# Optimization experiments

Measured on AMD Instinct MI355X. Metric: run time of the kernel, lower is better.

## Reference

```python
import jax, jax.numpy as jnp
import numpy as np

B, NQ, C, H, W, S1, S2 = 8, 100, 256, 64, 64, 7, 7
G = S1 * S2


def setup_inputs() -> dict:
    key = jax.random.key(0)
    ks = iter(jax.random.split(key, 64))
    rn = lambda shape, s=1.0: jax.random.normal(next(ks), shape, dtype=jnp.float32) * s
    d = {}
    d['q'] = rn((B, NQ, C))
    d['qpe'] = rn((B, NQ, C)) * 0.1
    d['feat'] = rn((B, C, H, W))
    d['feat_pe'] = rn((B, C, H, W)) * 0.1
    d['bboxes'] = jax.random.uniform(next(ks), (B, NQ, 4), dtype=jnp.float32)
    d['grid_embedding'] = rn((S1, S2, C), 0.02)
    for name in ['Wz', 'Wq', 'W1l', 'W2l', 'g1_w1', 'g1_w2', 'g2_w1', 'g2_w2',
                 'f1_w1', 'f1_w2', 'f2_w1', 'f2_w2', 'out_w']:
        d[name] = rn((C, C), 0.06)  # ~xavier for 256->256
    for name in ['bz', 'bq', 'b1l', 'b2l', 'g1_b1', 'g1_b2', 'g2_b1', 'g2_b2',
                 'f1_b1', 'f1_b2', 'f2_b1', 'f2_b2', 'out_b', 'g1_beta', 'g2_beta', 'out_beta']:
        d[name] = jnp.zeros((C,), jnp.float32)
    for name in ['g1_g', 'g2_g', 'out_g']:
        d[name] = jnp.ones((C,), jnp.float32)
    return d


def _ln(x, g, b):
    m = jnp.mean(x, -1, keepdims=True)
    v = jnp.mean((x - m) ** 2, -1, keepdims=True)
    return (x - m) * jax.lax.rsqrt(v + 1e-5) * g + b


def _mlp(x, w1, b1, w2, b2):  # 2-layer MLP: relu after first layer only
    return jax.nn.relu(x @ w1 + b1) @ w2 + b2


def _bilinear(img, gx, gy):
    # img: [B,C,H,W]; gx,gy: [B,P] in [-1,1]. torch grid_sample bilinear,
    # align_corners=False, zeros padding.
    Bb, Cc, Hh, Ww = img.shape
    ix = ((gx + 1.0) * Ww - 1.0) * 0.5
    iy = ((gy + 1.0) * Hh - 1.0) * 0.5
    x0 = jnp.floor(ix); x1 = x0 + 1.0
    y0 = jnp.floor(iy); y1 = y0 + 1.0
    wx1 = ix - x0; wx0 = 1.0 - wx1
    wy1 = iy - y0; wy0 = 1.0 - wy1
    flat = img.reshape(Bb, Cc, Hh * Ww)

    def tap(xf, yf):
        xi = xf.astype(jnp.int32); yi = yf.astype(jnp.int32)
        valid = (xi >= 0) & (xi < Ww) & (yi >= 0) & (yi < Hh)
        idx = jnp.clip(yi, 0, Hh - 1) * Ww + jnp.clip(xi, 0, Ww - 1)
        v = jnp.take_along_axis(flat, idx[:, None, :], axis=2)  # [B,C,P]
        return v * valid[:, None, :].astype(img.dtype)

    return (tap(x0, y0) * (wx0 * wy0)[:, None, :]
            + tap(x1, y0) * (wx1 * wy0)[:, None, :]
            + tap(x0, y1) * (wx0 * wy1)[:, None, :]
            + tap(x1, y1) * (wx1 * wy1)[:, None, :])


def _roi_sample(img, bboxes):
    # img: [B,C,H,W]; bboxes: [B,nq,4] xyhw -> returns [B,nq,G,C]
    Bb, Cc, Hh, Ww = img.shape
    nq = bboxes.shape[1]
    hs = jnp.arange(S1, dtype=img.dtype)
    ws = jnp.arange(S2, dtype=img.dtype)
    h_sl = bboxes[:, :, 2:3] / S1  # [B,nq,1]
    w_sl = bboxes[:, :, 3:4] / S2
    hh = h_sl * hs[None, None, :] + h_sl / 2.0  # [B,nq,S1]
    ww = w_sl * ws[None, None, :] + w_sl / 2.0  # [B,nq,S2]
    ys = jnp.broadcast_to(hh[:, :, :, None], (Bb, nq, S1, S2))
    xs = jnp.broadcast_to(ww[:, :, None, :], (Bb, nq, S1, S2))
    xs = xs + bboxes[:, :, 0, None, None] - bboxes[:, :, 3, None, None] / 2.0
    ys = ys + bboxes[:, :, 1, None, None] - bboxes[:, :, 2, None, None] / 2.0
    gx = jnp.clip(2.0 * xs - 1.0, -1.0, 1.0).reshape(Bb, -1)
    gy = jnp.clip(2.0 * ys - 1.0, -1.0, 1.0).reshape(Bb, -1)
    s = _bilinear(img, gx, gy)  # [B,C,nq*G]
    return s.reshape(Bb, Cc, nq, G).transpose(0, 2, 3, 1)  # [B,nq,G,C]


def reference(q, qpe, feat, feat_pe, bboxes, grid_embedding,
              Wz, bz, Wq, bq, W1l, b1l, W2l, b2l,
              g1_w1, g1_b1, g1_w2, g1_b2, g1_g, g1_beta,
              g2_w1, g2_b1, g2_w2, g2_b2, g2_g, g2_beta,
              f1_w1, f1_b1, f1_w2, f1_b2,
              f2_w1, f2_b1, f2_w2, f2_b2,
              out_w, out_b, out_g, out_beta):
    ge = grid_embedding.reshape(G, C)
    q_split = ((q + qpe) @ Wq + bq)[:, :, None, :] + ge[None, None]  # [B,nq,G,C]
    # 1x1 conv conv_z
    z = jnp.einsum('bchw,cd->bdhw', feat + feat_pe, Wz) + bz[None, :, None, None]
    roi_feat = _roi_sample(z, bboxes)  # [B,nq,G,C]
    k = (q_split @ W1l + b1l) * (roi_feat @ W2l + b2l)
    q2 = q[:, :, None, :] + ge[None, None]
    v = _roi_sample(feat, bboxes)  # [B,nq,G,C]
    gate1 = jax.nn.sigmoid(_ln(_mlp(k, g1_w1, g1_b1, g1_w2, g1_b2), g1_g, g1_beta))
    gate2 = jax.nn.sigmoid(_ln(_mlp(k, g2_w1, g2_b1, g2_w2, g2_b2), g2_g, g2_beta))
    out = gate1 * _mlp(q2, f1_w1, f1_b1, f1_w2, f1_b2) + gate2 * _mlp(v, f2_w1, f2_b1, f2_w2, f2_b2)
    return _ln(out @ out_w + out_b, out_g, out_beta)
```

## Files before the change

### kernel.cpp

```cpp
#include <hip/hip_runtime.h>
#include <hip/hip_bf16.h>
#include <hip/hip_fp8.h>

constexpr int Cc  = 256;
constexpr int NQ  = 100;
constexpr int Bb  = 8;
constexpr int HW  = 64 * 64;
constexpr int G49 = 49;

typedef __bf16 bf16x8 __attribute__((ext_vector_type(8)));
typedef float  f32x4  __attribute__((ext_vector_type(4)));

__device__ __forceinline__ float ldbf(const __hip_bfloat16* p) { return __bfloat162float(*p); }

__device__ __forceinline__ unsigned pk2(float a, float b) {
    union { unsigned u; __bf16 h[2]; } x;
    x.h[0] = (__bf16)a; x.h[1] = (__bf16)b;
    return x.u;
}
__device__ __forceinline__ float upk(unsigned u, int k) {
    union { unsigned u2; __bf16 h[2]; } x; x.u2 = u;
    return (float)x.h[k];
}
__device__ __forceinline__ float fp8lo(unsigned v) {
    union { unsigned char c; __hip_fp8_e4m3 f; } u; u.c = (unsigned char)(v & 255);
    return (float)u.f;
}
__device__ __forceinline__ float fp8hi(unsigned v) {
    union { unsigned char c; __hip_fp8_e4m3 f; } u; u.c = (unsigned char)((v >> 8) & 255);
    return (float)u.f;
}

__device__ __forceinline__ void lwb16(char* buf, int row, int col, float v) {
    int byte = (row * 512 + col * 2) ^ ((row & 7) << 4);
    *(__bf16*)(buf + byte) = (__bf16)v;
}

__global__ void prep1_kernel(const float* __restrict__ q, const float* __restrict__ qpe,
                             const float* __restrict__ ge,
                             const float* __restrict__ Wq, const float* __restrict__ bq,
                             const float* __restrict__ W1l, const float* __restrict__ b1l,
                             const float* __restrict__ f1_w1, const float* __restrict__ f1_b1,
                             __hip_bfloat16* __restrict__ qk1, __hip_bfloat16* __restrict__ qf1,
                             __hip_bfloat16* __restrict__ geW1, __hip_bfloat16* __restrict__ gef1)
{
    __shared__ float s[Cc];
    __shared__ float rq[Cc];
    __shared__ float qqs[Cc];
    const int t = threadIdx.x;
    const int blk = blockIdx.x;
    if (blk < Bb * NQ) {
        float a = q[blk * Cc + t], p = qpe[blk * Cc + t];
        rq[t] = a; s[t] = a + p;
        __syncthreads();
        float acc1 = bq[t], acc2 = f1_b1[t];
        for (int k = 0; k < Cc; k++) {
            acc1 = fmaf(s[k],  Wq[k * Cc + t],    acc1);
            acc2 = fmaf(rq[k], f1_w1[k * Cc + t], acc2);
        }
        qqs[t] = acc1;
        qf1[blk * Cc + t] = __float2bfloat16(acc2);
        __syncthreads();
        float acc3 = b1l[t];
        for (int k = 0; k < Cc; k++) acc3 = fmaf(qqs[k], W1l[k * Cc + t], acc3);
        qk1[blk * Cc + t] = __float2bfloat16(acc3);
    } else {
        int g = blk - Bb * NQ;
        s[t] = ge[g * Cc + t];
        __syncthreads();
        float acc1 = 0.f, acc2 = 0.f;
        for (int k = 0; k < Cc; k++) {
            acc1 = fmaf(s[k], W1l[k * Cc + t],   acc1);
            acc2 = fmaf(s[k], f1_w1[k * Cc + t], acc2);
        }
        geW1[g * Cc + t] = __float2bfloat16(acc1);
        gef1[g * Cc + t] = __float2bfloat16(acc2);
    }
}

__global__ void wfold_kernel(const float* __restrict__ Wz, const float* __restrict__ W2l,
                             const float* __restrict__ bz,
                             float* __restrict__ Wzc, float* __restrict__ bzW2l)
{
    __shared__ float s[Cc];
    const int t = threadIdx.x;
    const int blk = blockIdx.x;
    if (blk < Cc) {
        s[t] = Wz[blk * Cc + t];
        __syncthreads();
        float a = 0.f;
        for (int d = 0; d < Cc; d++) a = fmaf(s[d], W2l[d * Cc + t], a);
        Wzc[blk * Cc + t] = a;
    } else {
        s[t] = bz[t];
        __syncthreads();
        float a = 0.f;
        for (int d = 0; d < Cc; d++) a = fmaf(s[d], W2l[d * Cc + t], a);
        bzW2l[t] = a;
    }
}

__global__ void wprep_kernel(const float* __restrict__ Wzc,  const float* __restrict__ f2w1,
                             const float* __restrict__ g2w1, const float* __restrict__ g2w2,
                             const float* __restrict__ f2w2, const float* __restrict__ g1w1,
                             const float* __restrict__ g1w2, const float* __restrict__ f1w2,
                             const float* __restrict__ outw,
                             __hip_bfloat16* __restrict__ WTf)
{
    __shared__ float ld[64][65];
    const float* srcs[9] = {Wzc, f2w1, g2w1, g2w2, f2w2, g1w1, g1w2, f1w2, outw};
    const int m  = blockIdx.z;
    const int w  = blockIdx.y;
    const int k0 = blockIdx.x * 64;
    const float* src = srcs[m];
    __hip_bfloat16* dst = WTf + (size_t)m * 65536;
    const int t = threadIdx.x;
    const int n0 = w * 64;
#pragma unroll
    for (int j = 0; j < 16; j++) {
        int idx = j * 256 + t; int r = idx >> 6, c = idx & 63;
        ld[r][c] = src[(size_t)(k0 + r) * Cc + n0 + c];
    }
    __syncthreads();
#pragma unroll
    for (int j = 0; j < 16; j++) {
        int idx = j * 256 + t;
        int e  = idx & 7;
        int l  = (idx >> 3) & 63;
        int kk = (idx >> 9) & 1;
        int nt = idx >> 10;
        int k_loc = kk * 32 + ((l >> 4) & 3) * 8 + e;
        int n_loc = nt * 16 + (l & 15);
        int oofs  = ((w * 4 + nt) * 8 + (k0 >> 5) + kk) * 512 + (idx & 511);
        dst[oofs] = __float2bfloat16(ld[k_loc][n_loc]);
    }
}

__device__ __forceinline__ void run_gemm4(const char* __restrict__ Abuf,
                                          const __bf16* __restrict__ Wf,
                                          int l15, int lhi, int lane, int w, int n0, f32x4* acc)
{
#pragma unroll
    for (int j = 0; j < 16; j++) { f32x4 v = {0.f, 0.f, 0.f, 0.f}; acc[j] = v; }
#pragma unroll
    for (int ks = 0; ks < 8; ks++) {
        bf16x8 bfr[4], afr[4];
#pragma unroll
        for (int nt = 0; nt < 4; nt++)
            bfr[nt] = *(const bf16x8*)(Wf + ((((w * 4 + nt) * 8 + ks) * 64) + lane) * 8);
#pragma unroll
        for (int mt = 0; mt < 4; mt++) {
            int row = mt * 16 + l15;
            int byte = (row * 512 + (ks * 32 + lhi * 8) * 2) ^ ((row & 7) << 4);
            afr[mt] = *(const bf16x8*)(Abuf + byte);
        }
#pragma unroll
        for (int mt = 0; mt < 4; mt++)
#pragma unroll
            for (int nt = 0; nt < 4; nt++)
                acc[mt * 4 + nt] = __builtin_amdgcn_mfma_f32_16x16x32_bf16(
                    afr[mt], bfr[nt], acc[mt * 4 + nt], 0, 0, 0);
    }
}

__global__ __launch_bounds__(256, 2) void projA_kernel(
    const float* __restrict__ feat, const float* __restrict__ feat_pe,
    const __hip_bfloat16* __restrict__ WTf,
    __hip_fp8_e4m3* __restrict__ y1, __hip_bfloat16* __restrict__ y2)
{
    extern __shared__ char smem[];
    char* bufA = smem;
    char* bufB = smem + 32768;

    const int t = threadIdx.x;
    const int lane = t & 63;
    const int w = t >> 6;
    const int n0 = w * 64;
    const int l15 = lane & 15, lhi = lane >> 4;
    const int b = blockIdx.x >> 6;
    const int pix0 = (blockIdx.x & 63) * 64;

    const float* fp = feat    + ((size_t)(b * Cc + t)) * HW + pix0;
    const float* pp = feat_pe + ((size_t)(b * Cc + t)) * HW + pix0;
#pragma unroll
    for (int j = 0; j < 16; j++) {
        float4 f = *(const float4*)(fp + 4 * j);
        float4 p = *(const float4*)(pp + 4 * j);
        lwb16(bufB, 4 * j + 0, t, f.x); lwb16(bufA, 4 * j + 0, t, f.x + p.x);
        lwb16(bufB, 4 * j + 1, t, f.y); lwb16(bufA, 4 * j + 1, t, f.y + p.y);
        lwb16(bufB, 4 * j + 2, t, f.z); lwb16(bufA, 4 * j + 2, t, f.z + p.z);
        lwb16(bufB, 4 * j + 3, t, f.w); lwb16(bufA, 4 * j + 3, t, f.w + p.w);
    }
    __syncthreads();

    const __bf16* Wf_zc   = (const __bf16*)WTf + 0 * 65536;
    const __bf16* Wf_f2w1 = (const __bf16*)WTf + 1 * 65536;

    f32x4 acc[16];
    size_t base = ((size_t)b * HW + pix0) * Cc;

    run_gemm4(bufA, Wf_zc, l15, lhi, lane, w, n0, acc);
#pragma unroll
    for (int nt = 0; nt < 4; nt++)
#pragma unroll
        for (int mt = 0; mt < 4; mt++)
#pragma unroll
            for (int i = 0; i < 4; i++)
                y1[base + (size_t)(mt * 16 + lhi * 4 + i) * Cc + n0 + nt * 16 + l15] =
                    __hip_fp8_e4m3(acc[mt * 4 + nt][i]);

    run_gemm4(bufB, Wf_f2w1, l15, lhi, lane, w, n0, acc);
#pragma unroll
    for (int nt = 0; nt < 4; nt++)
#pragma unroll
        for (int mt = 0; mt < 4; mt++)
#pragma unroll
            for (int i = 0; i < 4; i++)
                y2[base + (size_t)(mt * 16 + lhi * 4 + i) * Cc + n0 + nt * 16 + l15] =
                    __float2bfloat16(acc[mt * 4 + nt][i]);
}

__device__ __forceinline__ void run_gemm8(const char* __restrict__ Abuf,
                                          const __bf16* __restrict__ Wf,
                                          const float* __restrict__ bias,
                                          int l15, int lhi, int lane, int wm, int wn, f32x4* acc)
{
#pragma unroll
    for (int nt = 0; nt < 4; nt++) {
        float bv = bias ? bias[wn * 64 + nt * 16 + l15] : 0.f;
        f32x4 v = {bv, bv, bv, bv};
        acc[0 * 4 + nt] = v; acc[1 * 4 + nt] = v;
    }
#pragma unroll
    for (int ks = 0; ks < 8; ks++) {
        bf16x8 bfr[4], afr[2];
#pragma unroll
        for (int nt = 0; nt < 4; nt++)
            bfr[nt] = *(const bf16x8*)(Wf + ((((wn * 4 + nt) * 8 + ks) * 64) + lane) * 8);
#pragma unroll
        for (int mt = 0; mt < 2; mt++) {
            int row = wm * 32 + mt * 16 + l15;
            int byte = (row * 512 + (ks * 32 + lhi * 8) * 2) ^ ((row & 7) << 4);
            afr[mt] = *(const bf16x8*)(Abuf + byte);
        }
        __builtin_amdgcn_s_setprio(1);
#pragma unroll
        for (int mt = 0; mt < 2; mt++)
#pragma unroll
            for (int nt = 0; nt < 4; nt++)
                acc[mt * 4 + nt] = __builtin_amdgcn_mfma_f32_16x16x32_bf16(
                    afr[mt], bfr[nt], acc[mt * 4 + nt], 0, 0, 0);
        __builtin_amdgcn_s_setprio(0);
    }
}

__device__ __forceinline__ void ln_stats8(const f32x4* acc, int l15, int lhi, int wm, int wn,
                                          int t, float* sred, float* smv)
{
    __syncthreads();
    float s[8], qq[8];
#pragma unroll
    for (int mt = 0; mt < 2; mt++)
#pragma unroll
        for (int i = 0; i < 4; i++) {
            float a = acc[mt * 4 + 0][i], b = acc[mt * 4 + 1][i];
            float c = acc[mt * 4 + 2][i], d = acc[mt * 4 + 3][i];
            s[mt * 4 + i]  = a + b + c + d;
            qq[mt * 4 + i] = a * a + b * b + c * c + d * d;
        }
#pragma unroll
    for (int off = 1; off < 16; off <<= 1)
#pragma unroll
        for (int j = 0; j < 8; j++) {
            s[j]  += __shfl_xor(s[j],  off);
            qq[j] += __shfl_xor(qq[j], off);
        }
    if (l15 == 0) {
#pragma unroll
        for (int mt = 0; mt < 2; mt++)
#pragma unroll
            for (int i = 0; i < 4; i++) {
                int row = wm * 32 + mt * 16 + lhi * 4 + i;
                sred[(row * 4 + wn) * 2]     = s[mt * 4 + i];
                sred[(row * 4 + wn) * 2 + 1] = qq[mt * 4 + i];
            }
    }
    __syncthreads();
    if (t < 64) {
        float ts = sred[(t * 4 + 0) * 2] + sred[(t * 4 + 1) * 2]
                 + sred[(t * 4 + 2) * 2] + sred[(t * 4 + 3) * 2];
        float tq = sred[(t * 4 + 0) * 2 + 1] + sred[(t * 4 + 1) * 2 + 1]
                 + sred[(t * 4 + 2) * 2 + 1] + sred[(t * 4 + 3) * 2 + 1];
        float m = ts * (1.f / 256.f);
        float var = fmaxf(tq * (1.f / 256.f) - m * m, 0.f);
        smv[t * 2]     = m;
        smv[t * 2 + 1] = rsqrtf(var + 1e-5f);
    }
    __syncthreads();
}

__device__ __forceinline__ void gate_apply8(const f32x4* acc, const float* __restrict__ g,
                                            const float* __restrict__ bet, const float* smv,
                                            int l15, int lhi, int wm, int wn, unsigned* gp)
{
#pragma unroll
    for (int nt = 0; nt < 4; nt++) {
        int col = wn * 64 + nt * 16 + l15;
        float gg = g[col], gb = bet[col];
#pragma unroll
        for (int mt = 0; mt < 2; mt++) {
            float gv[4];
#pragma unroll
            for (int i = 0; i < 4; i++) {
                int row = wm * 32 + mt * 16 + lhi * 4 + i;
                float u = (acc[mt * 4 + nt][i] - smv[row * 2]) * smv[row * 2 + 1] * gg + gb;
                gv[i] = 1.f / (1.f + __expf(-u));
            }
            gp[(mt * 4 + nt) * 2]     = pk2(gv[0], gv[1]);
            gp[(mt * 4 + nt) * 2 + 1] = pk2(gv[2], gv[3]);
        }
    }
}

__global__ __launch_bounds__(512, 2) void fused_kernel(
    const float* __restrict__ bboxes,
    const __hip_bfloat16* __restrict__ qk1, const __hip_bfloat16* __restrict__ qf1,
    const __hip_bfloat16* __restrict__ geW1, const __hip_bfloat16* __restrict__ gef1,
    const __hip_fp8_e4m3* __restrict__ y1, const __hip_bfloat16* __restrict__ y2,
    const __hip_bfloat16* __restrict__ WTf,
    const float* __restrict__ bzW2l, const float* __restrict__ b2l,
    const float* __restrict__ f2_b1, const float* __restrict__ f2_b2,
    const float* __restrict__ g1_b1, const float* __restrict__ g1_b2,
    const float* __restrict__ g1_g,  const float* __restrict__ g1_beta,
    const float* __restrict__ g2_b1, const float* __restrict__ g2_b2,
    const float* __restrict__ g2_g,  const float* __restrict__ g2_beta,
    const float* __restrict__ f1_b2,
    const float* __restrict__ out_b, const float* __restrict__ out_g,
    const float* __restrict__ out_beta,
    float* __restrict__ out)
{
    extern __shared__ char smem[];
    char* bufA = smem;
    char* bufB = smem + 32768;
    float* stg = (float*)smem;

    __shared__ int   ti[G49][4];
    __shared__ float tw[G49][4];
    __shared__ float tsw[G49];
    __shared__ float sred[64 * 4 * 2];
    __shared__ float smv[64 * 2];

    const int t = threadIdx.x;
    const int lane = t & 63;
    const int w = t >> 6;
    const int wm = w >> 2, wn = w & 3;
    const int l15 = lane & 15, lhi = lane >> 4;
    const int qid = (blockIdx.x & 7) * NQ + (blockIdx.x >> 3);
    const int b = blockIdx.x & 7;

    const __bf16* Wf_g2w1 = (const __bf16*)WTf + 2 * 65536;
    const __bf16* Wf_g2w2 = (const __bf16*)WTf + 3 * 65536;
    const __bf16* Wf_f2w2 = (const __bf16*)WTf + 4 * 65536;
    const __bf16* Wf_g1w1 = (const __bf16*)WTf + 5 * 65536;
    const __bf16* Wf_g1w2 = (const __bf16*)WTf + 6 * 65536;
    const __bf16* Wf_f1w2 = (const __bf16*)WTf + 7 * 65536;
    const __bf16* Wf_outw = (const __bf16*)WTf + 8 * 65536;

    if (t < G49) {
        float bb0 = bboxes[qid * 4 + 0];
        float bb1 = bboxes[qid * 4 + 1];
        float bb2 = bboxes[qid * 4 + 2];
        float bb3 = bboxes[qid * 4 + 3];
        int s1 = t / 7, s2 = t % 7;
        float ys = bb2 * (1.f / 7.f) * ((float)s1 + 0.5f) + bb1 - 0.5f * bb2;
        float xs = bb3 * (1.f / 7.f) * ((float)s2 + 0.5f) + bb0 - 0.5f * bb3;
        float gx = fminf(fmaxf(2.f * xs - 1.f, -1.f), 1.f);
        float gy = fminf(fmaxf(2.f * ys - 1.f, -1.f), 1.f);
        float ix = ((gx + 1.f) * 64.f - 1.f) * 0.5f;
        float iy = ((gy + 1.f) * 64.f - 1.f) * 0.5f;
        float x0f = floorf(ix), y0f = floorf(iy);
        float wx1 = ix - x0f, wx0 = 1.f - wx1;
        float wy1 = iy - y0f, wy0 = 1.f - wy1;
        int x0 = (int)x0f, y0 = (int)y0f;
        int x1 = x0 + 1, y1i = y0 + 1;
        bool vx0 = (x0 >= 0) & (x0 < 64), vx1 = (x1 >= 0) & (x1 < 64);
        bool vy0 = (y0 >= 0) & (y0 < 64), vy1 = (y1i >= 0) & (y1i < 64);
        int cx0 = min(max(x0, 0), 63), cx1 = min(max(x1, 0), 63);
        int cy0 = min(max(y0, 0), 63), cy1 = min(max(y1i, 0), 63);
        float w0 = (vx0 && vy0) ? wx0 * wy0 : 0.f;
        float w1 = (vx1 && vy0) ? wx1 * wy0 : 0.f;
        float w2 = (vx0 && vy1) ? wx0 * wy1 : 0.f;
        float w3 = (vx1 && vy1) ? wx1 * wy1 : 0.f;
        ti[t][0] = cy0 * 64 + cx0; tw[t][0] = w0;
        ti[t][1] = cy0 * 64 + cx1; tw[t][1] = w1;
        ti[t][2] = cy1 * 64 + cx0; tw[t][2] = w2;
        ti[t][3] = cy1 * 64 + cx1; tw[t][3] = w3;
        tsw[t] = w0 + w1 + w2 + w3;
    }
    if (t < Cc) {
        for (int r = G49; r < 64; r++) { lwb16(bufA, r, t, 0.f); lwb16(bufB, r, t, 0.f); }
    }
    __syncthreads();

    {
        const __hip_fp8_e4m3* y1b = y1 + (size_t)b * HW * Cc;
        const __hip_bfloat16* y2b = y2 + (size_t)b * HW * Cc;
        const int c2 = (t & 127) * 2;
        const int rs = t >> 7;
        const float qk0  = ldbf(&qk1[qid * Cc + c2]);
        const float qk1v = ldbf(&qk1[qid * Cc + c2 + 1]);
        const float bzw0 = bzW2l[c2],  bzw1 = bzW2l[c2 + 1];
        const float b20  = b2l[c2],    b21  = b2l[c2 + 1];
        const float fb0  = f2_b1[c2],  fb1  = f2_b1[c2 + 1];
        for (int it = 0; it < 13; it++) {
            int r = it * 4 + rs;
            if (r < G49) {
                int4   tix = *(const int4*)&ti[r][0];
                float4 twx = *(const float4*)&tw[r][0];
                size_t o0 = (size_t)tix.x * Cc + c2;
                size_t o1 = (size_t)tix.y * Cc + c2;
                size_t o2 = (size_t)tix.z * Cc + c2;
                size_t o3 = (size_t)tix.w * Cc + c2;
                unsigned p0 = *(const unsigned short*)((const char*)y1b + o0);
                unsigned p1 = *(const unsigned short*)((const char*)y1b + o1);
                unsigned p2 = *(const unsigned short*)((const char*)y1b + o2);
                unsigned p3 = *(const unsigned short*)((const char*)y1b + o3);
                unsigned q0 = *(const unsigned*)(y2b + o0);
                unsigned q1 = *(const unsigned*)(y2b + o1);
                unsigned q2 = *(const unsigned*)(y2b + o2);
                unsigned q3 = *(const unsigned*)(y2b + o3);
                float a10 = fp8lo(p0) * twx.x + fp8lo(p1) * twx.y
                          + fp8lo(p2) * twx.z + fp8lo(p3) * twx.w;
                float a11 = fp8hi(p0) * twx.x + fp8hi(p1) * twx.y
                          + fp8hi(p2) * twx.z + fp8hi(p3) * twx.w;
                float a20 = upk(q0, 0) * twx.x + upk(q1, 0) * twx.y
                          + upk(q2, 0) * twx.z + upk(q3, 0) * twx.w;
                float a21 = upk(q0, 1) * twx.x + upk(q1, 1) * twx.y
                          + upk(q2, 1) * twx.z + upk(q3, 1) * twx.w;
                float ts_ = tsw[r];
                unsigned gep = *(const unsigned*)(geW1 + r * Cc + c2);
                float kv0 = (qk0  + upk(gep, 0)) * (a10 + ts_ * bzw0 + b20);
                float kv1 = (qk1v + upk(gep, 1)) * (a11 + ts_ * bzw1 + b21);
                int byteB = (r * 512 + c2 * 2) ^ ((r & 7) << 4);
                *(unsigned*)(bufB + byteB) = pk2(kv0, kv1);
                *(unsigned*)(bufA + byteB) = pk2(fmaxf(a20 + fb0, 0.f), fmaxf(a21 + fb1, 0.f));
            }
        }
    }
    __syncthreads();

    f32x4 acc[8], acc2[8];

    run_gemm8(bufA, Wf_f2w2, f2_b2, l15, lhi, lane, wm, wn, acc);
    unsigned m2p[16];
#pragma unroll
    for (int j = 0; j < 8; j++) {
        m2p[j * 2]     = pk2(acc[j][0], acc[j][1]);
        m2p[j * 2 + 1] = pk2(acc[j][2], acc[j][3]);
    }

    run_gemm8(bufB, Wf_g2w1, g2_b1, l15, lhi, lane, wm, wn, acc);
    run_gemm8(bufB, Wf_g1w1, g1_b1, l15, lhi, lane, wm, wn, acc2);
    __syncthreads();
#pragma unroll
    for (int nt = 0; nt < 4; nt++)
#pragma unroll
        for (int mt = 0; mt < 2; mt++)
#pragma unroll
            for (int i = 0; i < 4; i++) {
                int row = wm * 32 + mt * 16 + lhi * 4 + i, col = wn * 64 + nt * 16 + l15;
                lwb16(bufA, row, col, fmaxf(acc [mt * 4 + nt][i], 0.f));
                lwb16(bufB, row, col, fmaxf(acc2[mt * 4 + nt][i], 0.f));
            }
    __syncthreads();

    run_gemm8(bufA, Wf_g2w2, g2_b2, l15, lhi, lane, wm, wn, acc);
    ln_stats8(acc, l15, lhi, wm, wn, t, sred, smv);
    unsigned g2p[16];
    gate_apply8(acc, g2_g, g2_beta, smv, l15, lhi, wm, wn, g2p);
    unsigned comb[16];
#pragma unroll
    for (int j = 0; j < 16; j++)
        comb[j] = pk2(upk(g2p[j], 0) * upk(m2p[j], 0), upk(g2p[j], 1) * upk(m2p[j], 1));

    run_gemm8(bufB, Wf_g1w2, g1_b2, l15, lhi, lane, wm, wn, acc);
    ln_stats8(acc, l15, lhi, wm, wn, t, sred, smv);
    unsigned g1p[16];
    gate_apply8(acc, g1_g, g1_beta, smv, l15, lhi, wm, wn, g1p);

    {
        int col = t & 255, rh = t >> 8;
        float qf = ldbf(&qf1[qid * Cc + col]);
        for (int it = 0; it < 32; it++) {
            int r = it * 2 + rh;
            int rr = r < G49 ? r : 0;
            lwb16(bufA, r, col, fmaxf(qf + ldbf(&gef1[rr * Cc + col]), 0.f));
        }
    }
    __syncthreads();

    run_gemm8(bufA, Wf_f1w2, f1_b2, l15, lhi, lane, wm, wn, acc);
    __syncthreads();
#pragma unroll
    for (int nt = 0; nt < 4; nt++)
#pragma unroll
        for (int mt = 0; mt < 2; mt++)
#pragma unroll
            for (int i = 0; i < 4; i++) {
                int j = mt * 4 + nt;
                int hw_ = i >> 1, lo = i & 1;
                float f = upk(comb[j * 2 + hw_], lo) + upk(g1p[j * 2 + hw_], lo) * acc[j][i];
                lwb16(bufA, wm * 32 + mt * 16 + lhi * 4 + i, wn * 64 + nt * 16 + l15, f);
            }
    __syncthreads();

    run_gemm8(bufA, Wf_outw, out_b, l15, lhi, lane, wm, wn, acc);
    ln_stats8(acc, l15, lhi, wm, wn, t, sred, smv);
#pragma unroll
    for (int nt = 0; nt < 4; nt++) {
        int col = wn * 64 + nt * 16 + l15;
        float gg = out_g[col], gb = out_beta[col];
#pragma unroll
        for (int mt = 0; mt < 2; mt++)
#pragma unroll
            for (int i = 0; i < 4; i++) {
                int row = wm * 32 + mt * 16 + lhi * 4 + i;
                if (row < G49)
                    stg[row * Cc + col] =
                        (acc[mt * 4 + nt][i] - smv[row * 2]) * smv[row * 2 + 1] * gg + gb;
            }
    }
    __syncthreads();
    {
        float* ob = out + (size_t)qid * G49 * Cc;
#pragma unroll
        for (int it = 0; it < 7; it++) {
            int fid = it * 512 + t;
            int r = fid >> 6, c4 = (fid & 63) * 4;
            if (r < G49) {
                f32x4 v = *(const f32x4*)&stg[r * Cc + c4];
                *(f32x4*)&ob[r * Cc + c4] = v;
            }
        }
    }
}

extern "C" void kernel_launch(void* const* d_in, const int* in_sizes, int n_in,
                              void* d_out, int out_size, void* d_ws, size_t ws_size,
                              hipStream_t stream)
{
    const float* q       = (const float*)d_in[0];
    const float* qpe     = (const float*)d_in[1];
    const float* feat    = (const float*)d_in[2];
    const float* feat_pe = (const float*)d_in[3];
    const float* bboxes  = (const float*)d_in[4];
    const float* ge      = (const float*)d_in[5];
    const float* Wz      = (const float*)d_in[6];
    const float* Wq      = (const float*)d_in[7];
    const float* W1l     = (const float*)d_in[8];
    const float* W2l     = (const float*)d_in[9];
    const float* g1_w1   = (const float*)d_in[10];
    const float* g1_w2   = (const float*)d_in[11];
    const float* g2_w1   = (const float*)d_in[12];
    const float* g2_w2   = (const float*)d_in[13];
    const float* f1_w1   = (const float*)d_in[14];
    const float* f1_w2   = (const float*)d_in[15];
    const float* f2_w1   = (const float*)d_in[16];
    const float* f2_w2   = (const float*)d_in[17];
    const float* out_w   = (const float*)d_in[18];
    const float* bz      = (const float*)d_in[19];
    const float* bq      = (const float*)d_in[20];
    const float* b1l     = (const float*)d_in[21];
    const float* b2l     = (const float*)d_in[22];
    const float* g1_b1   = (const float*)d_in[23];
    const float* g1_b2   = (const float*)d_in[24];
    const float* g2_b1   = (const float*)d_in[25];
    const float* g2_b2   = (const float*)d_in[26];
    const float* f1_b1   = (const float*)d_in[27];
    const float* f1_b2   = (const float*)d_in[28];
    const float* f2_b1   = (const float*)d_in[29];
    const float* f2_b2   = (const float*)d_in[30];
    const float* out_b   = (const float*)d_in[31];
    const float* g1_beta = (const float*)d_in[32];
    const float* g2_beta = (const float*)d_in[33];
    const float* out_beta= (const float*)d_in[34];
    const float* g1_g    = (const float*)d_in[35];
    const float* g2_g    = (const float*)d_in[36];
    const float* out_g   = (const float*)d_in[37];

    char* ws = (char*)d_ws;
    __hip_bfloat16* qk1   = (__hip_bfloat16*)(ws);
    __hip_bfloat16* qf1   = (__hip_bfloat16*)(ws + 409600);
    __hip_bfloat16* geW1  = (__hip_bfloat16*)(ws + 819200);
    __hip_bfloat16* gef1  = (__hip_bfloat16*)(ws + 844288);
    float*          bzW2l = (float*)(ws + 869376);
    float*          WzcF  = (float*)(ws + 870400);
    __hip_bfloat16* WTf   = (__hip_bfloat16*)(ws + 1132544);
    __hip_fp8_e4m3* y1    = (__hip_fp8_e4m3*)(ws + 2312192);
    __hip_bfloat16* y2    = (__hip_bfloat16*)(ws + 10700800);

    prep1_kernel<<<dim3(Bb * NQ + G49), dim3(256), 0, stream>>>(
        q, qpe, ge, Wq, bq, W1l, b1l, f1_w1, f1_b1, qk1, qf1, geW1, gef1);

    wfold_kernel<<<dim3(Cc + 1), dim3(256), 0, stream>>>(Wz, W2l, bz, WzcF, bzW2l);

    wprep_kernel<<<dim3(4, 4, 9), dim3(256), 0, stream>>>(
        WzcF, f2_w1, g2_w1, g2_w2, f2_w2, g1_w1, g1_w2, f1_w2, out_w, WTf);

    projA_kernel<<<dim3(512), dim3(256), 65536, stream>>>(feat, feat_pe, WTf, y1, y2);

    fused_kernel<<<dim3(Bb * NQ), dim3(512), 65536, stream>>>(
        bboxes, qk1, qf1, geW1, gef1, y1, y2, WTf,
        bzW2l, b2l, f2_b1, f2_b2,
        g1_b1, g1_b2, g1_g, g1_beta,
        g2_b1, g2_b2, g2_g, g2_beta,
        f1_b2, out_b, out_g, out_beta, (float*)d_out);
}
```

Measured before the change: 257.4 us.

## Pack two queries per 1024-thread block in fused kernel

The fused kernel now runs two queries per block, with 1024 threads split into two independent 512-thread halves. Each half gets its own 64KB dynamic shared memory region and its own sampling and LayerNorm scratch. The grid is halved, and the shared-memory limit is raised to 128KB through a one-time attribute call. The aim is to change scheduling and occupancy and share block-level overhead across queries, but the block-wide __syncthreads now couples the two halves, and launch bounds of (1024,1) may change register allocation.

New measurement: 314.8 us. +22.3%, slower.

```diff
diff --git a/kernel.cpp b/kernel.cpp
--- a/kernel.cpp
+++ b/kernel.cpp
@@ -255,7 +255,7 @@
 }
 
 __device__ __forceinline__ void ln_stats8(const f32x4* acc, int l15, int lhi, int wm, int wn,
-                                          int t, float* sred, float* smv)
+                                          int tl, float* sred, float* smv)
 {
     __syncthreads();
     float s[8], qq[8];
@@ -286,15 +286,15 @@
             }
     }
     __syncthreads();
-    if (t < 64) {
-        float ts = sred[(t * 4 + 0) * 2] + sred[(t * 4 + 1) * 2]
-                 + sred[(t * 4 + 2) * 2] + sred[(t * 4 + 3) * 2];
-        float tq = sred[(t * 4 + 0) * 2 + 1] + sred[(t * 4 + 1) * 2 + 1]
-                 + sred[(t * 4 + 2) * 2 + 1] + sred[(t * 4 + 3) * 2 + 1];
+    if (tl < 64) {
+        float ts = sred[(tl * 4 + 0) * 2] + sred[(tl * 4 + 1) * 2]
+                 + sred[(tl * 4 + 2) * 2] + sred[(tl * 4 + 3) * 2];
+        float tq = sred[(tl * 4 + 0) * 2 + 1] + sred[(tl * 4 + 1) * 2 + 1]
+                 + sred[(tl * 4 + 2) * 2 + 1] + sred[(tl * 4 + 3) * 2 + 1];
         float m = ts * (1.f / 256.f);
         float var = fmaxf(tq * (1.f / 256.f) - m * m, 0.f);
-        smv[t * 2]     = m;
-        smv[t * 2 + 1] = rsqrtf(var + 1e-5f);
+        smv[tl * 2]     = m;
+        smv[tl * 2 + 1] = rsqrtf(var + 1e-5f);
     }
     __syncthreads();
 }
@@ -322,7 +322,7 @@
     }
 }
 
-__global__ __launch_bounds__(512, 2) void fused_kernel(
+__global__ __launch_bounds__(1024, 1) void fused_kernel(
     const float* __restrict__ bboxes,
     const __hip_bfloat16* __restrict__ qk1, const __hip_bfloat16* __restrict__ qf1,
     const __hip_bfloat16* __restrict__ geW1, const __hip_bfloat16* __restrict__ gef1,
@@ -340,23 +340,25 @@
     float* __restrict__ out)
 {
     extern __shared__ char smem[];
-    char* bufA = smem;
-    char* bufB = smem + 32768;
-    float* stg = (float*)smem;
-
-    __shared__ int   ti[G49][4];
-    __shared__ float tw[G49][4];
-    __shared__ float tsw[G49];
-    __shared__ float sred[64 * 4 * 2];
-    __shared__ float smv[64 * 2];
-
     const int t = threadIdx.x;
+    const int half = t >> 9;
+    const int tl = t & 511;
+    char*  bufA = smem + half * 65536;
+    char*  bufB = bufA + 32768;
+    float* stg  = (float*)(smem + half * 65536);
+
+    __shared__ int   ti[2][G49][4];
+    __shared__ float tw[2][G49][4];
+    __shared__ float tsw[2][G49];
+    __shared__ float sred[2][64 * 4 * 2];
+    __shared__ float smv[2][64 * 2];
+
     const int lane = t & 63;
-    const int w = t >> 6;
+    const int w = tl >> 6;
     const int wm = w >> 2, wn = w & 3;
     const int l15 = lane & 15, lhi = lane >> 4;
-    const int qid = (blockIdx.x & 7) * NQ + (blockIdx.x >> 3);
     const int b = blockIdx.x & 7;
+    const int qid = b * NQ + ((blockIdx.x >> 3) * 2) + half;
 
     const __bf16* Wf_g2w1 = (const __bf16*)WTf + 2 * 65536;
     const __bf16* Wf_g2w2 = (const __bf16*)WTf + 3 * 65536;
@@ -366,12 +368,12 @@
     const __bf16* Wf_f1w2 = (const __bf16*)WTf + 7 * 65536;
     const __bf16* Wf_outw = (const __bf16*)WTf + 8 * 65536;
 
-    if (t < G49) {
+    if (tl < G49) {
         float bb0 = bboxes[qid * 4 + 0];
         float bb1 = bboxes[qid * 4 + 1];
         float bb2 = bboxes[qid * 4 + 2];
         float bb3 = bboxes[qid * 4 + 3];
-        int s1 = t / 7, s2 = t % 7;
+        int s1 = tl / 7, s2 = tl % 7;
         float ys = bb2 * (1.f / 7.f) * ((float)s1 + 0.5f) + bb1 - 0.5f * bb2;
         float xs = bb3 * (1.f / 7.f) * ((float)s2 + 0.5f) + bb0 - 0.5f * bb3;
         float gx = fminf(fmaxf(2.f * xs - 1.f, -1.f), 1.f);
@@ -391,22 +393,22 @@
         float w1 = (vx1 && vy0) ? wx1 * wy0 : 0.f;
         float w2 = (vx0 && vy1) ? wx0 * wy1 : 0.f;
         float w3 = (vx1 && vy1) ? wx1 * wy1 : 0.f;
-        ti[t][0] = cy0 * 64 + cx0; tw[t][0] = w0;
-        ti[t][1] = cy0 * 64 + cx1; tw[t][1] = w1;
-        ti[t][2] = cy1 * 64 + cx0; tw[t][2] = w2;
-        ti[t][3] = cy1 * 64 + cx1; tw[t][3] = w3;
-        tsw[t] = w0 + w1 + w2 + w3;
-    }
-    if (t < Cc) {
-        for (int r = G49; r < 64; r++) { lwb16(bufA, r, t, 0.f); lwb16(bufB, r, t, 0.f); }
+        ti[half][tl][0] = cy0 * 64 + cx0; tw[half][tl][0] = w0;
+        ti[half][tl][1] = cy0 * 64 + cx1; tw[half][tl][1] = w1;
+        ti[half][tl][2] = cy1 * 64 + cx0; tw[half][tl][2] = w2;
+        ti[half][tl][3] = cy1 * 64 + cx1; tw[half][tl][3] = w3;
+        tsw[half][tl] = w0 + w1 + w2 + w3;
+    }
+    if (tl < Cc) {
+        for (int r = G49; r < 64; r++) { lwb16(bufA, r, tl, 0.f); lwb16(bufB, r, tl, 0.f); }
     }
     __syncthreads();
 
     {
         const __hip_fp8_e4m3* y1b = y1 + (size_t)b * HW * Cc;
         const __hip_bfloat16* y2b = y2 + (size_t)b * HW * Cc;
-        const int c2 = (t & 127) * 2;
-        const int rs = t >> 7;
+        const int c2 = (tl & 127) * 2;
+        const int rs = tl >> 7;
         const float qk0  = ldbf(&qk1[qid * Cc + c2]);
         const float qk1v = ldbf(&qk1[qid * Cc + c2 + 1]);
         const float bzw0 = bzW2l[c2],  bzw1 = bzW2l[c2 + 1];
@@ -415,8 +417,8 @@
         for (int it = 0; it < 13; it++) {
             int r = it * 4 + rs;
             if (r < G49) {
-                int4   tix = *(const int4*)&ti[r][0];
-                float4 twx = *(const float4*)&tw[r][0];
+                int4   tix = *(const int4*)&ti[half][r][0];
+                float4 twx = *(const float4*)&tw[half][r][0];
                 size_t o0 = (size_t)tix.x * Cc + c2;
                 size_t o1 = (size_t)tix.y * Cc + c2;
                 size_t o2 = (size_t)tix.z * Cc + c2;
@@ -437,7 +439,7 @@
                           + upk(q2, 0) * twx.z + upk(q3, 0) * twx.w;
                 float a21 = upk(q0, 1) * twx.x + upk(q1, 1) * twx.y
                           + upk(q2, 1) * twx.z + upk(q3, 1) * twx.w;
-                float ts_ = tsw[r];
+                float ts_ = tsw[half][r];
                 unsigned gep = *(const unsigned*)(geW1 + r * Cc + c2);
                 float kv0 = (qk0  + upk(gep, 0)) * (a10 + ts_ * bzw0 + b20);
                 float kv1 = (qk1v + upk(gep, 1)) * (a11 + ts_ * bzw1 + b21);
@@ -475,21 +477,21 @@
     __syncthreads();
 
     run_gemm8(bufA, Wf_g2w2, g2_b2, l15, lhi, lane, wm, wn, acc);
-    ln_stats8(acc, l15, lhi, wm, wn, t, sred, smv);
+    ln_stats8(acc, l15, lhi, wm, wn, tl, sred[half], smv[half]);
     unsigned g2p[16];
-    gate_apply8(acc, g2_g, g2_beta, smv, l15, lhi, wm, wn, g2p);
+    gate_apply8(acc, g2_g, g2_beta, smv[half], l15, lhi, wm, wn, g2p);
     unsigned comb[16];
 #pragma unroll
     for (int j = 0; j < 16; j++)
         comb[j] = pk2(upk(g2p[j], 0) * upk(m2p[j], 0), upk(g2p[j], 1) * upk(m2p[j], 1));
 
     run_gemm8(bufB, Wf_g1w2, g1_b2, l15, lhi, lane, wm, wn, acc);
-    ln_stats8(acc, l15, lhi, wm, wn, t, sred, smv);
+    ln_stats8(acc, l15, lhi, wm, wn, tl, sred[half], smv[half]);
     unsigned g1p[16];
-    gate_apply8(acc, g1_g, g1_beta, smv, l15, lhi, wm, wn, g1p);
+    gate_apply8(acc, g1_g, g1_beta, smv[half], l15, lhi, wm, wn, g1p);
 
     {
-        int col = t & 255, rh = t >> 8;
+        int col = tl & 255, rh = tl >> 8;
         float qf = ldbf(&qf1[qid * Cc + col]);
         for (int it = 0; it < 32; it++) {
             int r = it * 2 + rh;
@@ -515,7 +517,7 @@
     __syncthreads();
 
     run_gemm8(bufA, Wf_outw, out_b, l15, lhi, lane, wm, wn, acc);
-    ln_stats8(acc, l15, lhi, wm, wn, t, sred, smv);
+    ln_stats8(acc, l15, lhi, wm, wn, tl, sred[half], smv[half]);
 #pragma unroll
     for (int nt = 0; nt < 4; nt++) {
         int col = wn * 64 + nt * 16 + l15;
@@ -527,7 +529,7 @@
                 int row = wm * 32 + mt * 16 + lhi * 4 + i;
                 if (row < G49)
                     stg[row * Cc + col] =
-                        (acc[mt * 4 + nt][i] - smv[row * 2]) * smv[row * 2 + 1] * gg + gb;
+                        (acc[mt * 4 + nt][i] - smv[half][row * 2]) * smv[half][row * 2 + 1] * gg + gb;
             }
     }
     __syncthreads();
@@ -535,7 +537,7 @@
         float* ob = out + (size_t)qid * G49 * Cc;
 #pragma unroll
         for (int it = 0; it < 7; it++) {
-            int fid = it * 512 + t;
+            int fid = it * 512 + tl;
             int r = fid >> 6, c4 = (fid & 63) * 4;
             if (r < G49) {
                 f32x4 v = *(const f32x4*)&stg[r * Cc + c4];
@@ -599,6 +601,13 @@
     __hip_fp8_e4m3* y1    = (__hip_fp8_e4m3*)(ws + 2312192);
     __hip_bfloat16* y2    = (__hip_bfloat16*)(ws + 10700800);
 
+    static bool attr_set = false;
+    if (!attr_set) {
+        (void)hipFuncSetAttribute((const void*)fused_kernel,
+                                  hipFuncAttributeMaxDynamicSharedMemorySize, 131072);
+        attr_set = true;
+    }
+
     prep1_kernel<<<dim3(Bb * NQ + G49), dim3(256), 0, stream>>>(
         q, qpe, ge, Wq, bq, W1l, b1l, f1_w1, f1_b1, qk1, qf1, geW1, gef1);
 
@@ -609,7 +618,7 @@
 
     projA_kernel<<<dim3(512), dim3(256), 65536, stream>>>(feat, feat_pe, WTf, y1, y2);
 
-    fused_kernel<<<dim3(Bb * NQ), dim3(512), 65536, stream>>>(
+    fused_kernel<<<dim3(Bb * NQ / 2), dim3(1024), 131072, stream>>>(
         bboxes, qk1, qf1, geW1, gef1, y1, y2, WTf,
         bzW2l, b2l, f2_b1, f2_b2,
         g1_b1, g1_b2, g1_g, g1_beta,
```
